# Kernel optimization log

Measured on AMD Instinct MI355X. Metric: run time of the kernel, lower is better.

## Reference

```python
import jax, jax.numpy as jnp
import numpy as np
from jax import lax

B, C, H, W = 16, 3, 512, 512


def _nms(heat):
    # 3x3 max-pool, stride 1, SAME padding; keep only local peaks
    hmax = lax.reduce_window(heat, -jnp.inf, lax.max,
                             (1, 1, 3, 3), (1, 1, 1, 1), 'SAME')
    return heat * (hmax == heat).astype(heat.dtype)


def _topk(scores, K):
    b, c, h, w = scores.shape
    # per-class topk over the spatial plane
    topk_scores, topk_inds = lax.top_k(scores.reshape(b, c, h * w), K)  # [b,c,K]
    topk_row = (topk_inds // w).astype(scores.dtype)
    topk_col = (topk_inds % w).astype(scores.dtype)
    # global topk across (class, K)
    topk_score, topk_ind = lax.top_k(topk_scores.reshape(b, c * K), K)  # [b,K]
    topk_clses = topk_ind // K
    gath = lambda x: jnp.take_along_axis(x.reshape(b, c * K), topk_ind, axis=1)
    return topk_score, gath(topk_inds), topk_clses, gath(topk_row), gath(topk_col)


def _transpose_and_gather_feat(feat, inds):
    b, ch, h, w = feat.shape
    f = feat.transpose(0, 2, 3, 1).reshape(b, h * w, ch)  # [b,HW,ch]
    return jnp.take_along_axis(f, inds[:, :, None], axis=1)  # [b,K,ch]


def _decode(hm, cen_offset, direction, z_coor, dim, K):
    b = hm.shape[0]
    hm = _nms(hm)
    scores, inds, clses, row, col = _topk(hm, K)
    off = _transpose_and_gather_feat(cen_offset, inds)           # [b,K,2]
    col = col[:, :, None] + off[:, :, 0:1]
    row = row[:, :, None] + off[:, :, 1:2]
    direction = _transpose_and_gather_feat(direction, inds)      # [b,K,2]
    z_coor = _transpose_and_gather_feat(z_coor, inds)            # [b,K,1]
    dim = _transpose_and_gather_feat(dim, inds)                  # [b,K,3]
    clses = clses[:, :, None].astype(hm.dtype)
    scores = scores[:, :, None]
    return jnp.concatenate([scores, col, row, z_coor, dim, direction, clses], axis=2)


def setup_inputs() -> dict:
    key = jax.random.key(0)
    k1, k2, k3, k4, k5 = jax.random.split(key, 5)
    return {
        'hm_cen': jax.random.normal(k1, (B, C, H, W), jnp.float32),
        'cen_offset': jax.random.normal(k2, (B, 2, H, W), jnp.float32),
        'direction': jax.random.normal(k3, (B, 2, H, W), jnp.float32),
        'z_coor': jax.random.normal(k4, (B, 1, H, W), jnp.float32),
        'dim': jax.random.normal(k5, (B, 3, H, W), jnp.float32),
        'K': 500,
    }


def reference(hm_cen, cen_offset, direction, z_coor, dim, K):
    # postprocessing_v2 applies sigmoid to the class heatmap before decode
    heat = jax.nn.sigmoid(hm_cen)
    return _decode(heat, cen_offset, direction, z_coor, dim, K)  # [B,K,10]
```

## Files before the change

kernel.cpp:

```cpp
#include <hip/hip_runtime.h>
#include <math.h>
#include <float.h>

#define Hd 512
#define Wd 512
#define HWp (Hd*Wd)
#define Bn 16
#define Cn 3
#define NMAP (Bn*Cn)
#define KTOP 500
#define PBANDS 16
#define BAND 32
#define CAPB 4096

__device__ __forceinline__ uint32_t flipbits(float v){
  uint32_t u = __float_as_uint(v);
  return u ^ (0x80000000u | (uint32_t)(-(int32_t)(u>>31)));
}
__device__ __forceinline__ float unflipbits(uint32_t f){
  uint32_t u = f ^ ((f>>31)? 0x80000000u : 0xFFFFFFFFu);
  return __uint_as_float(u);
}

__device__ __forceinline__ void nms_row(
    const float4 p0, const float4 p1, const float4 c0, const float4 c1,
    const float4 n0, const float4 n1, const int lane,
    uint32_t& pk, float* cv)
{
  float vm0 = fmaxf(fmaxf(p0.x,c0.x),n0.x);
  float vm1 = fmaxf(fmaxf(p0.y,c0.y),n0.y);
  float vm2 = fmaxf(fmaxf(p0.z,c0.z),n0.z);
  float vm3 = fmaxf(fmaxf(p0.w,c0.w),n0.w);
  float vm4 = fmaxf(fmaxf(p1.x,c1.x),n1.x);
  float vm5 = fmaxf(fmaxf(p1.y,c1.y),n1.y);
  float vm6 = fmaxf(fmaxf(p1.z,c1.z),n1.z);
  float vm7 = fmaxf(fmaxf(p1.w,c1.w),n1.w);
  float vmL = __shfl_up(vm7, 1);   if (lane == 0)  vmL = -INFINITY;
  float vmR = __shfl_down(vm0, 1); if (lane == 63) vmR = -INFINITY;

  float m0 = fmaxf(vmL, fmaxf(vm0, vm1));
  float m1 = fmaxf(vm0, fmaxf(vm1, vm2));
  float m2 = fmaxf(vm1, fmaxf(vm2, vm3));
  float m3 = fmaxf(vm2, fmaxf(vm3, vm4));
  float m4 = fmaxf(vm3, fmaxf(vm4, vm5));
  float m5 = fmaxf(vm4, fmaxf(vm5, vm6));
  float m6 = fmaxf(vm5, fmaxf(vm6, vm7));
  float m7 = fmaxf(vm6, fmaxf(vm7, vmR));

  pk = 0;
  if (c0.x >= m0) pk |= 1u;
  if (c0.y >= m1) pk |= 2u;
  if (c0.z >= m2) pk |= 4u;
  if (c0.w >= m3) pk |= 8u;
  if (c1.x >= m4) pk |= 16u;
  if (c1.y >= m5) pk |= 32u;
  if (c1.z >= m6) pk |= 64u;
  if (c1.w >= m7) pk |= 128u;
  cv[0]=c0.x; cv[1]=c0.y; cv[2]=c0.z; cv[3]=c0.w;
  cv[4]=c1.x; cv[5]=c1.y; cv[6]=c1.z; cv[7]=c1.w;
}

__global__ __launch_bounds__(512) void k_nms(
    const float* __restrict__ hm, uint64_t* __restrict__ seg_all,
    uint32_t* __restrict__ cnt)
{
  __shared__ uint32_t ctr;
  const int bid = blockIdx.x;
  const int m = bid >> 4, p = bid & (PBANDS - 1);
  const int tid = threadIdx.x, lane = tid & 63, w = tid >> 6;
  const float* map = hm + (size_t)m * HWp;
  uint64_t* dst = seg_all + (size_t)bid * CAPB;
  const int y0 = p * BAND + w * 4;
  const int xb = lane * 8;

  if (tid == 0) ctr = 0;
  __syncthreads();

  const float4 NEG4 = make_float4(-INFINITY,-INFINITY,-INFINITY,-INFINITY);
  float4 ra[6], rb[6];
  #pragma unroll
  for (int r = 0; r < 6; ++r) {
    const int yy = y0 - 1 + r;
    if (yy >= 0 && yy < Hd) {
      const float* rp = map + (size_t)yy * Wd + xb;
      ra[r] = *(const float4*)rp; rb[r] = *(const float4*)(rp + 4);
    } else { ra[r] = NEG4; rb[r] = NEG4; }
  }

  #pragma unroll
  for (int r = 0; r < 4; ++r) {
    uint32_t pk; float cv[8];
    nms_row(ra[r], rb[r], ra[r+1], rb[r+1], ra[r+2], rb[r+2], lane, pk, cv);
    const uint32_t np = (uint32_t)__popc(pk);
    uint32_t incl = np;
    #pragma unroll
    for (int d = 1; d < 64; d <<= 1) { uint32_t u = __shfl_up(incl, d); if (lane >= d) incl += u; }
    const uint32_t tot = __shfl(incl, 63);
    if (!tot) continue;
    uint32_t b0 = 0;
    if (lane == 0) b0 = atomicAdd(&ctr, tot);
    b0 = __shfl(b0, 0);
    uint32_t pos = b0 + incl - np;
    const uint32_t ib = (uint32_t)((y0 + r) * Wd + xb);
    #pragma unroll
    for (int i = 0; i < 8; ++i) {
      if ((pk >> i) & 1u) {
        if (pos < (uint32_t)CAPB)
          dst[pos] = ((uint64_t)flipbits(cv[i]) << 32) | (uint32_t)(~(ib + (uint32_t)i));
        ++pos;
      }
    }
  }
  __syncthreads();
  if (tid == 0) cnt[bid] = (ctr < (uint32_t)CAPB) ? ctr : (uint32_t)CAPB;
}

__device__ __forceinline__ void findT4096(
    const uint32_t* hist, const uint32_t target, const int tid, const int lane,
    const int wid, uint32_t* wtot, uint32_t* res)
{
  const uint32_t s = hist[4*tid] + hist[4*tid+1] + hist[4*tid+2] + hist[4*tid+3];
  uint32_t v = s;
  #pragma unroll
  for (int d = 1; d < 64; d <<= 1) { uint32_t u = __shfl_down(v, d); if (lane + d < 64) v += u; }
  if (lane == 0) wtot[wid] = v;
  __syncthreads();
  uint32_t above = 0;
  for (int ww = wid + 1; ww < 16; ++ww) above += wtot[ww];
  const uint32_t gsuf = v + above;
  if (gsuf >= target && (gsuf - s) < target) {
    uint32_t cum = gsuf - s;
    for (int b = 4*tid + 3; b >= 4*tid; --b) {
      cum += hist[b];
      if (cum >= target) { res[0]=(uint32_t)b; res[1]=target-(cum-hist[b]); res[2]=cum; break; }
    }
  }
  __syncthreads();
}

__global__ __launch_bounds__(1024) void k_select(
    const uint64_t* __restrict__ seg_all, const uint32_t* __restrict__ cnt,
    float* __restrict__ s1_scores, uint32_t* __restrict__ s1_inds)
{
  __shared__ uint32_t hist[4096];
  __shared__ uint64_t csel[1024];
  __shared__ uint32_t wtot[16];
  __shared__ uint32_t res[4];

  const int m = blockIdx.x;
  const int tid = threadIdx.x, lane = tid & 63, wid = tid >> 6;
  const uint64_t lt = (1ull << lane) - 1ull;

  for (int i = tid; i < 4096; i += 1024) hist[i] = 0;
  if (tid == 0) res[3] = 0;
  __syncthreads();

  const uint64_t* sg = seg_all + (size_t)(m * PBANDS + wid) * CAPB;
  const uint32_t sn = min(cnt[m * PBANDS + wid], (uint32_t)CAPB);

  for (uint32_t base = 0; base < sn; base += 256u) {
    const uint32_t i0 = base + (uint32_t)lane, i1 = i0 + 64u, i2 = i0 + 128u, i3 = i0 + 192u;
    uint64_t k0 = 0, k1 = 0, k2 = 0, k3 = 0;
    if (i0 < sn) k0 = sg[i0];
    if (i1 < sn) k1 = sg[i1];
    if (i2 < sn) k2 = sg[i2];
    if (i3 < sn) k3 = sg[i3];
    if (i0 < sn) atomicAdd(&hist[(uint32_t)(k0 >> 52)], 1u);
    if (i1 < sn) atomicAdd(&hist[(uint32_t)(k1 >> 52)], 1u);
    if (i2 < sn) atomicAdd(&hist[(uint32_t)(k2 >> 52)], 1u);
    if (i3 < sn) atomicAdd(&hist[(uint32_t)(k3 >> 52)], 1u);
  }
  __syncthreads();

  findT4096(hist, KTOP, tid, lane, wid, wtot, res);
  const uint32_t T1 = res[0], krem = res[1], M0 = res[2];
  __syncthreads();

  uint32_t shift = 20, thr = T1;
  if (M0 > 1024u) {
    for (int i = tid; i < 4096; i += 1024) hist[i] = 0;
    __syncthreads();
    for (uint32_t i = (uint32_t)lane; i < sn; i += 64u) {
      const uint32_t f = (uint32_t)(sg[i] >> 32);
      if ((f >> 20) == T1) atomicAdd(&hist[(f >> 8) & 4095u], 1u);
    }
    __syncthreads();
    findT4096(hist, krem, tid, lane, wid, wtot, res);
    shift = 8; thr = (T1 << 12) | res[0];
    __syncthreads();
  }

  for (uint32_t base = 0; base < sn; base += 256u) {
    const uint32_t i0 = base + (uint32_t)lane, i1 = i0 + 64u, i2 = i0 + 128u, i3 = i0 + 192u;
    uint64_t k0 = 0, k1 = 0, k2 = 0, k3 = 0;
    if (i0 < sn) k0 = sg[i0];
    if (i1 < sn) k1 = sg[i1];
    if (i2 < sn) k2 = sg[i2];
    if (i3 < sn) k3 = sg[i3];
    const bool p0 = (i0 < sn) && (((uint32_t)(k0 >> 32) >> shift) >= thr);
    const bool p1 = (i1 < sn) && (((uint32_t)(k1 >> 32) >> shift) >= thr);
    const bool p2 = (i2 < sn) && (((uint32_t)(k2 >> 32) >> shift) >= thr);
    const bool p3 = (i3 < sn) && (((uint32_t)(k3 >> 32) >> shift) >= thr);
    #define APP(K, P) {                                                  \
      const unsigned long long mask = __ballot(P);                       \
      if (mask) {                                                        \
        uint32_t b = 0;                                                  \
        if (lane == 0) b = atomicAdd(&res[3], (uint32_t)__popcll(mask)); \
        b = __shfl(b, 0);                                                \
        if (P) {                                                         \
          const uint32_t pp = b + (uint32_t)__popcll(mask & lt);         \
          if (pp < 1024u) csel[pp] = K;                                  \
        }                                                                \
      }                                                                  \
    }
    APP(k0, p0) APP(k1, p1) APP(k2, p2) APP(k3, p3)
    #undef APP
  }
  __syncthreads();
  uint32_t M = res[3]; if (M > 1024u) M = 1024u;
  const uint32_t Mp = (M + 3u) & ~3u;
  if ((uint32_t)tid >= M && (uint32_t)tid < Mp) csel[tid] = 0ull;
  __syncthreads();

  const uint64_t kk = ((uint32_t)tid < M) ? csel[tid] : 0ull;
  uint32_t rank = 0;
  for (uint32_t j = 0; j < Mp; j += 4u) {
    rank += (csel[j]   > kk) ? 1u : 0u;
    rank += (csel[j+1] > kk) ? 1u : 0u;
    rank += (csel[j+2] > kk) ? 1u : 0u;
    rank += (csel[j+3] > kk) ? 1u : 0u;
  }
  if ((uint32_t)tid < M && rank < 512u) {
    const float v = unflipbits((uint32_t)(kk >> 32));
    s1_scores[m * 512 + rank] = 1.0f / (1.0f + expf(-v));
    s1_inds [m * 512 + rank] = ~(uint32_t)kk;
  }
  if ((uint32_t)tid >= M && tid < 512) {
    s1_scores[m * 512 + tid] = 0.0f;
    s1_inds [m * 512 + tid] = 0u;
  }
}

__global__ __launch_bounds__(512) void k_final(
    const float* __restrict__ s1_scores, const uint32_t* __restrict__ s1_inds,
    const float* __restrict__ cen_offset, const float* __restrict__ direction,
    const float* __restrict__ z_coor, const float* __restrict__ dimf,
    float* __restrict__ out)
{
  __shared__ float ssc[Cn][KTOP];
  const int b = blockIdx.x / Cn, c = blockIdx.x % Cn;
  const int tid = threadIdx.x;

  for (int i = tid; i < Cn * KTOP; i += 512) {
    int cc = i / KTOP, r = i - cc * KTOP;
    ssc[cc][r] = s1_scores[(b * Cn + cc) * 512 + r];
  }
  __syncthreads();

  if (tid < KTOP) {
    const int r = tid;
    const int i = c * KTOP + r;
    const uint64_t mykey = ((uint64_t)flipbits(ssc[c][r]) << 32) | (uint32_t)(~(uint32_t)i);
    int rank = r;
    #pragma unroll
    for (int cd = 1; cd < Cn; ++cd) {
      const int cc = (c + cd) % Cn;
      int lo = 0, hi = KTOP;
      while (lo < hi) {
        int mid = (lo + hi) >> 1;
        uint64_t k2 = ((uint64_t)flipbits(ssc[cc][mid]) << 32)
                    | (uint32_t)(~(uint32_t)(cc * KTOP + mid));
        if (k2 > mykey) lo = mid + 1; else hi = mid;
      }
      rank += lo;
    }
    if (rank < KTOP) {
      const float* co = cen_offset + (size_t)b * 2 * HWp;
      const float* di = direction  + (size_t)b * 2 * HWp;
      const float* zc = z_coor     + (size_t)b * HWp;
      const float* dm = dimf       + (size_t)b * 3 * HWp;
      const int bcx = b * Cn + c;
      const uint32_t ind = s1_inds[bcx * 512 + r];
      float o[10];
      o[0] = ssc[c][r];
      o[1] = (float)(ind & (Wd - 1)) + co[ind];
      o[2] = (float)(ind >> 9) + co[HWp + ind];
      o[3] = zc[ind];
      o[4] = dm[ind];
      o[5] = dm[HWp + ind];
      o[6] = dm[2 * HWp + ind];
      o[7] = di[ind];
      o[8] = di[HWp + ind];
      o[9] = (float)c;
      float* op = out + ((size_t)b * KTOP + rank) * 10;
      #pragma unroll
      for (int q = 0; q < 10; ++q) op[q] = o[q];
    }
  }
}

extern "C" void kernel_launch(void* const* d_in, const int* in_sizes, int n_in,
                              void* d_out, int out_size, void* d_ws, size_t ws_size,
                              hipStream_t stream)
{
  const float* hm         = (const float*)d_in[0];
  const float* cen_offset = (const float*)d_in[1];
  const float* direction  = (const float*)d_in[2];
  const float* z_coor     = (const float*)d_in[3];
  const float* dimf       = (const float*)d_in[4];
  float* out = (float*)d_out;

  char* ws = (char*)d_ws;
  uint32_t* cnt   = (uint32_t*)ws;
  float*    s1_sc = (float*)(ws + 4096);
  uint32_t* s1_id = (uint32_t*)(ws + 4096 + (size_t)NMAP * 512 * 4);
  size_t fixed    = 4096 + (size_t)NMAP * 512 * 4 * 2;
  uint64_t* seg   = (uint64_t*)(ws + fixed);

  k_nms   <<<NMAP * PBANDS, 512, 0, stream>>>(hm, seg, cnt);
  k_select<<<NMAP,         1024, 0, stream>>>(seg, cnt, s1_sc, s1_id);
  k_final <<<Bn * Cn,       512, 0, stream>>>(s1_sc, s1_id, cen_offset, direction, z_coor, dimf, out);
}
```

Baseline: 61.61 us.

## Build radix histogram in NMS kernel and replace rank sort with bitonic sort

The NMS kernel now builds a 4096-bin histogram of the top 12 bits of each peak's key in shared memory and merges it atomically into a per-map global histogram. This lets the select kernel skip its first pass over all candidates. The select kernel also raises the candidate buffer to 2048, so the second refinement pass runs less often, and replaces the O(M^2) rank counting with a bitonic sort. The cost is a memset of the global histogram, extra shared-memory atomics in NMS, and many syncthreads inside the bitonic stages.

```diff
diff --git a/kernel.cpp b/kernel.cpp
--- a/kernel.cpp
+++ b/kernel.cpp
@@ -62,8 +62,9 @@
 
 __global__ __launch_bounds__(512) void k_nms(
     const float* __restrict__ hm, uint64_t* __restrict__ seg_all,
-    uint32_t* __restrict__ cnt)
-{
+    uint32_t* __restrict__ cnt, uint32_t* __restrict__ ghist)
+{
+  __shared__ uint32_t lhist[4096];
   __shared__ uint32_t ctr;
   const int bid = blockIdx.x;
   const int m = bid >> 4, p = bid & (PBANDS - 1);
@@ -73,6 +74,7 @@
   const int y0 = p * BAND + w * 4;
   const int xb = lane * 8;
 
+  for (int i = tid; i < 4096; i += 512) lhist[i] = 0;
   if (tid == 0) ctr = 0;
   __syncthreads();
 
@@ -105,14 +107,21 @@
     #pragma unroll
     for (int i = 0; i < 8; ++i) {
       if ((pk >> i) & 1u) {
+        const uint32_t fb = flipbits(cv[i]);
         if (pos < (uint32_t)CAPB)
-          dst[pos] = ((uint64_t)flipbits(cv[i]) << 32) | (uint32_t)(~(ib + (uint32_t)i));
+          dst[pos] = ((uint64_t)fb << 32) | (uint32_t)(~(ib + (uint32_t)i));
+        atomicAdd(&lhist[fb >> 20], 1u);
         ++pos;
       }
     }
   }
   __syncthreads();
   if (tid == 0) cnt[bid] = (ctr < (uint32_t)CAPB) ? ctr : (uint32_t)CAPB;
+  uint32_t* gh = ghist + (size_t)m * 4096;
+  for (int i = tid; i < 4096; i += 512) {
+    const uint32_t v = lhist[i];
+    if (v) atomicAdd(&gh[i], v);
+  }
 }
 
 __device__ __forceinline__ void findT4096(
@@ -138,12 +147,74 @@
   __syncthreads();
 }
 
+__device__ __forceinline__ uint64_t cexch(uint64_t mine, uint64_t part, bool wantMax) {
+  uint64_t mx = mine > part ? mine : part;
+  uint64_t mn = mine > part ? part : mine;
+  return wantMax ? mx : mn;
+}
+
+__device__ void bitonic1024_1t(uint64_t& e0, uint64_t* sbuf, int tid, int lane)
+{
+  for (int k = 2; k <= 1024; k <<= 1) {
+    for (int j = k >> 1; j > 0; j >>= 1) {
+      const bool up = ((tid & k) == 0);
+      if (j >= 64) {
+        __syncthreads();
+        sbuf[tid] = e0;
+        __syncthreads();
+        uint64_t q = sbuf[tid ^ j];
+        e0 = cexch(e0, q, up == ((tid & j) == 0));
+      } else {
+        uint64_t q = __shfl_xor((unsigned long long)e0, j);
+        e0 = cexch(e0, q, up == ((lane & j) == 0));
+      }
+    }
+  }
+  __syncthreads();
+  sbuf[tid] = e0;
+  __syncthreads();
+}
+
+__device__ void bitonic2048_reg(uint64_t& e0, uint64_t& e1, uint64_t* sbuf, int tid, int lane)
+{
+  const int i1 = tid + 1024;
+  for (int k = 2; k <= 2048; k <<= 1) {
+    for (int j = k >> 1; j > 0; j >>= 1) {
+      if (j >= 1024) {
+        uint64_t mx = e0 > e1 ? e0 : e1;
+        uint64_t mn = e0 > e1 ? e1 : e0;
+        e0 = mx; e1 = mn;
+      } else if (j >= 64) {
+        __syncthreads();
+        sbuf[tid] = e0; sbuf[i1] = e1;
+        __syncthreads();
+        uint64_t q0 = sbuf[tid ^ j];
+        uint64_t q1 = sbuf[i1 ^ j];
+        bool amS = ((tid & j) == 0);
+        e0 = cexch(e0, q0, ((tid & k) == 0) == amS);
+        e1 = cexch(e1, q1, ((i1  & k) == 0) == amS);
+      } else {
+        uint64_t q0 = __shfl_xor((unsigned long long)e0, j);
+        uint64_t q1 = __shfl_xor((unsigned long long)e1, j);
+        bool amS = ((lane & j) == 0);
+        e0 = cexch(e0, q0, ((tid & k) == 0) == amS);
+        e1 = cexch(e1, q1, ((i1  & k) == 0) == amS);
+      }
+    }
+  }
+  __syncthreads();
+  sbuf[tid] = e0; sbuf[i1] = e1;
+  __syncthreads();
+}
+
 __global__ __launch_bounds__(1024) void k_select(
     const uint64_t* __restrict__ seg_all, const uint32_t* __restrict__ cnt,
+    const uint32_t* __restrict__ ghist,
     float* __restrict__ s1_scores, uint32_t* __restrict__ s1_inds)
 {
   __shared__ uint32_t hist[4096];
-  __shared__ uint64_t csel[1024];
+  __shared__ uint64_t csel[2048];
+  __shared__ uint32_t segn[16];
   __shared__ uint32_t wtot[16];
   __shared__ uint32_t res[4];
 
@@ -151,43 +222,37 @@
   const int tid = threadIdx.x, lane = tid & 63, wid = tid >> 6;
   const uint64_t lt = (1ull << lane) - 1ull;
 
-  for (int i = tid; i < 4096; i += 1024) hist[i] = 0;
+  for (int i = tid; i < 4096; i += 1024) hist[i] = ghist[(size_t)m * 4096 + i];
+  if (tid < 16) segn[tid] = min(cnt[m * PBANDS + tid], (uint32_t)CAPB);
   if (tid == 0) res[3] = 0;
   __syncthreads();
 
+  uint32_t n = 0;
+  #pragma unroll
+  for (int s = 0; s < 16; ++s) n += segn[s];
+
   const uint64_t* sg = seg_all + (size_t)(m * PBANDS + wid) * CAPB;
-  const uint32_t sn = min(cnt[m * PBANDS + wid], (uint32_t)CAPB);
-
-  for (uint32_t base = 0; base < sn; base += 256u) {
-    const uint32_t i0 = base + (uint32_t)lane, i1 = i0 + 64u, i2 = i0 + 128u, i3 = i0 + 192u;
-    uint64_t k0 = 0, k1 = 0, k2 = 0, k3 = 0;
-    if (i0 < sn) k0 = sg[i0];
-    if (i1 < sn) k1 = sg[i1];
-    if (i2 < sn) k2 = sg[i2];
-    if (i3 < sn) k3 = sg[i3];
-    if (i0 < sn) atomicAdd(&hist[(uint32_t)(k0 >> 52)], 1u);
-    if (i1 < sn) atomicAdd(&hist[(uint32_t)(k1 >> 52)], 1u);
-    if (i2 < sn) atomicAdd(&hist[(uint32_t)(k2 >> 52)], 1u);
-    if (i3 < sn) atomicAdd(&hist[(uint32_t)(k3 >> 52)], 1u);
-  }
-  __syncthreads();
-
-  findT4096(hist, KTOP, tid, lane, wid, wtot, res);
-  const uint32_t T1 = res[0], krem = res[1], M0 = res[2];
-  __syncthreads();
-
-  uint32_t shift = 20, thr = T1;
-  if (M0 > 1024u) {
-    for (int i = tid; i < 4096; i += 1024) hist[i] = 0;
+  const uint32_t sn = segn[wid];
+
+  uint32_t shift = 20, thr = 0;
+  if (n > 512) {
+    findT4096(hist, KTOP, tid, lane, wid, wtot, res);
+    const uint32_t T1 = res[0], krem = res[1], M0 = res[2];
     __syncthreads();
-    for (uint32_t i = (uint32_t)lane; i < sn; i += 64u) {
-      const uint32_t f = (uint32_t)(sg[i] >> 32);
-      if ((f >> 20) == T1) atomicAdd(&hist[(f >> 8) & 4095u], 1u);
-    }
-    __syncthreads();
-    findT4096(hist, krem, tid, lane, wid, wtot, res);
-    shift = 8; thr = (T1 << 12) | res[0];
-    __syncthreads();
+    if (M0 <= 2048u) {
+      thr = T1;
+    } else {
+      for (int i = tid; i < 4096; i += 1024) hist[i] = 0;
+      __syncthreads();
+      for (uint32_t i = (uint32_t)lane; i < sn; i += 64u) {
+        const uint32_t f = (uint32_t)(sg[i] >> 32);
+        if ((f >> 20) == T1) atomicAdd(&hist[(f >> 8) & 4095u], 1u);
+      }
+      __syncthreads();
+      findT4096(hist, krem, tid, lane, wid, wtot, res);
+      shift = 8; thr = (T1 << 12) | res[0];
+      __syncthreads();
+    }
   }
 
   for (uint32_t base = 0; base < sn; base += 256u) {
@@ -209,7 +274,7 @@
         b = __shfl(b, 0);                                                \
         if (P) {                                                         \
           const uint32_t pp = b + (uint32_t)__popcll(mask & lt);         \
-          if (pp < 1024u) csel[pp] = K;                                  \
+          if (pp < 2048u) csel[pp] = K;                                  \
         }                                                                \
       }                                                                  \
     }
@@ -217,27 +282,29 @@
     #undef APP
   }
   __syncthreads();
-  uint32_t M = res[3]; if (M > 1024u) M = 1024u;
-  const uint32_t Mp = (M + 3u) & ~3u;
-  if ((uint32_t)tid >= M && (uint32_t)tid < Mp) csel[tid] = 0ull;
-  __syncthreads();
-
-  const uint64_t kk = ((uint32_t)tid < M) ? csel[tid] : 0ull;
-  uint32_t rank = 0;
-  for (uint32_t j = 0; j < Mp; j += 4u) {
-    rank += (csel[j]   > kk) ? 1u : 0u;
-    rank += (csel[j+1] > kk) ? 1u : 0u;
-    rank += (csel[j+2] > kk) ? 1u : 0u;
-    rank += (csel[j+3] > kk) ? 1u : 0u;
-  }
-  if ((uint32_t)tid < M && rank < 512u) {
-    const float v = unflipbits((uint32_t)(kk >> 32));
-    s1_scores[m * 512 + rank] = 1.0f / (1.0f + expf(-v));
-    s1_inds [m * 512 + rank] = ~(uint32_t)kk;
-  }
-  if ((uint32_t)tid >= M && tid < 512) {
-    s1_scores[m * 512 + tid] = 0.0f;
-    s1_inds [m * 512 + tid] = 0u;
+  uint32_t M = res[3]; if (M > 2048u) M = 2048u;
+  for (uint32_t i = M + (uint32_t)tid; i < 2048u; i += 1024u) csel[i] = 0ull;
+  __syncthreads();
+
+  if (M <= 1024u) {
+    uint64_t e0 = csel[tid];
+    bitonic1024_1t(e0, csel, tid, lane);
+  } else {
+    uint64_t e0 = csel[tid], e1 = csel[tid + 1024];
+    bitonic2048_reg(e0, e1, csel, tid, lane);
+  }
+
+  if (tid < 512) {
+    const uint64_t kk = csel[tid];
+    float score; uint32_t idx;
+    if (kk == 0ull) { score = 0.0f; idx = 0u; }
+    else {
+      idx = ~(uint32_t)kk;
+      const float v = unflipbits((uint32_t)(kk >> 32));
+      score = 1.0f / (1.0f + expf(-v));
+    }
+    s1_scores[m * 512 + tid] = score;
+    s1_inds [m * 512 + tid] = idx;
   }
 }
 
@@ -311,13 +378,16 @@
   float* out = (float*)d_out;
 
   char* ws = (char*)d_ws;
-  uint32_t* cnt   = (uint32_t*)ws;
-  float*    s1_sc = (float*)(ws + 4096);
-  uint32_t* s1_id = (uint32_t*)(ws + 4096 + (size_t)NMAP * 512 * 4);
-  size_t fixed    = 4096 + (size_t)NMAP * 512 * 4 * 2;
+  uint32_t* ghist = (uint32_t*)ws;
+  size_t o0       = (size_t)NMAP * 4096 * 4;
+  uint32_t* cnt   = (uint32_t*)(ws + o0);
+  float*    s1_sc = (float*)(ws + o0 + 4096);
+  uint32_t* s1_id = (uint32_t*)(ws + o0 + 4096 + (size_t)NMAP * 512 * 4);
+  size_t fixed    = o0 + 4096 + (size_t)NMAP * 512 * 4 * 2;
   uint64_t* seg   = (uint64_t*)(ws + fixed);
 
-  k_nms   <<<NMAP * PBANDS, 512, 0, stream>>>(hm, seg, cnt);
-  k_select<<<NMAP,         1024, 0, stream>>>(seg, cnt, s1_sc, s1_id);
+  hipMemsetAsync(ghist, 0, o0, stream);
+  k_nms   <<<NMAP * PBANDS, 512, 0, stream>>>(hm, seg, cnt, ghist);
+  k_select<<<NMAP,         1024, 0, stream>>>(seg, cnt, ghist, s1_sc, s1_id);
   k_final <<<Bn * Cn,       512, 0, stream>>>(s1_sc, s1_id, cen_offset, direction, z_coor, dimf, out);
 }
```

Result: faster. 54.14 us (-12.1%).
